# Performance work log

Measured on AMD Instinct MI355X. Metric: run time of the kernel, lower is better.

The kernel has to match this reference:

```python
import jax, jax.numpy as jnp
import numpy as np

A_MIN = 0.001
EPS = 1e-08


def setup_inputs() -> dict:
    key = jax.random.key(0)
    k1, k2, k3, k4 = jax.random.split(key, 4)
    B, O, I = 512, 1024, 512
    x = jax.random.normal(k1, (B, I), dtype=jnp.float32)
    translation = jax.random.uniform(k2, (O, I), dtype=jnp.float32, minval=-1.0, maxval=1.0)
    scale_raw = jax.random.uniform(k3, (O, I), dtype=jnp.float32, minval=-2.0, maxval=0.0)
    weights = jax.random.normal(k4, (O, I), dtype=jnp.float32) * (1.0 / np.sqrt(I))
    return {"x": x, "translation": translation, "scale_raw": scale_raw, "weights": weights}


def reference(x, translation, scale_raw, weights):
    # x: (B, I); params: (O, I)
    scale = A_MIN + jax.nn.softplus(scale_raw)  # (O, I)
    # s: (B, O, I) broadcast intermediate
    s = (x[:, None, :] - translation[None, :, :]) / (scale[None, :, :] + EPS)
    s2 = s * s
    wavelet = (1.0 - s2) * jnp.exp(-0.5 * s2)  # mexican hat
    y = jnp.einsum('oi,boi->bo', weights, wavelet)  # reduce over in_features
    return y
```

## Files before the change

kernel.cpp:

```cpp
#include <hip/hip_runtime.h>


#define WL_A_MIN 0.001f
#define WL_EPS   1e-8f

constexpr int WL_B = 512;
constexpr int WL_O = 1024;
constexpr int WL_I = 512;

#define WL_SQK  0.84932180553704583800f
#define WL_IK   1.38629436111989061883f
#define WL_L2E  1.44269504088896340736f
#define WL_LN2  0.69314718055994530942f

typedef float v2f __attribute__((ext_vector_type(2)));

struct P3 { float nti, inv, w; };

__device__ __forceinline__ float fast_exp2(float a) {
#if __has_builtin(__builtin_amdgcn_exp2f)
    return __builtin_amdgcn_exp2f(a);
#else
    return exp2f(a);
#endif
}
__device__ __forceinline__ float fast_log2(float a) {
#if __has_builtin(__builtin_amdgcn_logf)
    return __builtin_amdgcn_logf(a);
#else
    return __log2f(a);
#endif
}
__device__ __forceinline__ float fast_rcp(float a) {
#if __has_builtin(__builtin_amdgcn_rcpf)
    return __builtin_amdgcn_rcpf(a);
#else
    return 1.0f / a;
#endif
}

__global__ __launch_bounds__(256) void wl_prep(
    const float* __restrict__ translation,
    const float* __restrict__ scale_raw,
    const float* __restrict__ weights,
    v2f* __restrict__ A2,
    float* __restrict__ W1)
{
    __shared__ P3 lds[16 * 64];
    const int t  = threadIdx.x;
    const int o0 = blockIdx.x * 64;
    const int i0 = blockIdx.y * 16;

    {
        const int o_l = t >> 2;
        const int iq  = t & 3;
        const size_t g = (size_t)(o0 + o_l) * WL_I + (i0 + iq * 4);
        const float4 tv = *reinterpret_cast<const float4*>(translation + g);
        const float4 sv = *reinterpret_cast<const float4*>(scale_raw   + g);
        const float4 wv = *reinterpret_cast<const float4*>(weights     + g);
        const float tt[4] = {tv.x, tv.y, tv.z, tv.w};
        const float ss[4] = {sv.x, sv.y, sv.z, sv.w};
        const float ww[4] = {wv.x, wv.y, wv.z, wv.w};
        #pragma unroll
        for (int j = 0; j < 4; ++j) {
            float ex  = fast_exp2(ss[j] * WL_L2E);
            float sp  = fast_log2(1.0f + ex) * WL_LN2;
            float inv = fast_rcp(WL_A_MIN + sp + WL_EPS) * WL_SQK;
            P3 pv; pv.nti = -tt[j] * inv; pv.inv = inv; pv.w = ww[j];
            lds[(iq * 4 + j) * 64 + o_l] = pv;
        }
    }
    __syncthreads();
    {
        const int o_l = t & 63;
        const int r   = t >> 6;
        const int o   = o0 + o_l;
        #pragma unroll
        for (int j = 0; j < 4; ++j) {
            const int i_l = r * 4 + j;
            P3 a = lds[i_l * 64 + o_l];
            A2[(size_t)(i0 + i_l) * WL_O + o] = (v2f){a.nti, a.inv};
            W1[(size_t)(i0 + i_l) * WL_O + o] = a.w;
        }
    }
}

__global__ __launch_bounds__(1024, 8) void wl_main(
    const float* __restrict__ x,
    const v2f* __restrict__ A2,
    const float* __restrict__ W1,
    float* __restrict__ out)
{
    __shared__ float smem[8192];

    const int tid  = threadIdx.x;
    const int lane = tid & 63;
    const int wid  = tid >> 6;
    const int o    = blockIdx.x * 64 + lane;
    const int b0   = blockIdx.y * 16;

    {
        const int b_l = tid & 15;
        const int seg = tid >> 4;
        const float* xg = &x[(size_t)(b0 + b_l) * WL_I + seg * 8];
        const float4 v0 = *reinterpret_cast<const float4*>(xg);
        const float4 v1 = *reinterpret_cast<const float4*>(xg + 4);
        const int base = seg * 8 * 16 + b_l;
        smem[base + 0 * 16] = v0.x;
        smem[base + 1 * 16] = v0.y;
        smem[base + 2 * 16] = v0.z;
        smem[base + 3 * 16] = v0.w;
        smem[base + 4 * 16] = v1.x;
        smem[base + 5 * 16] = v1.y;
        smem[base + 6 * 16] = v1.z;
        smem[base + 7 * 16] = v1.w;
    }
    __syncthreads();

    const v2f*   __restrict__ pA = A2 + (size_t)(wid * 32) * WL_O + o;
    const float* __restrict__ pW = W1 + (size_t)(wid * 32) * WL_O + o;
    const float* xrow = &smem[wid * 32 * 16];

    float acc[16] = {0.f,0.f,0.f,0.f, 0.f,0.f,0.f,0.f,
                     0.f,0.f,0.f,0.f, 0.f,0.f,0.f,0.f};

    #pragma unroll 4
    for (int ii = 0; ii < 32; ++ii) {
        const v2f   pa = pA[(size_t)ii * WL_O];
        const float w  = pW[(size_t)ii * WL_O];
        const float mwk = w * (-WL_IK);
        const float nti = pa.x, inv = pa.y;
        const float4* xf = reinterpret_cast<const float4*>(xrow + ii * 16);
        #pragma unroll
        for (int q = 0; q < 4; ++q) {
            const float4 xq = xf[q];
            const float xs[4] = {xq.x, xq.y, xq.z, xq.w};
            #pragma unroll
            for (int j = 0; j < 4; ++j) {
                const int b = q * 4 + j;
                const float s = fmaf(xs[j], inv, nti);
                const float u = s * s;
                const float e = fast_exp2(-u);
                const float v = fmaf(mwk, u, w);
                acc[b] = fmaf(v, e, acc[b]);
            }
        }
    }

    __syncthreads();
    #pragma unroll
    for (int k = 0; k < 8; ++k)
        smem[(wid * 8 + k) * 64 + lane] = acc[k];
    __syncthreads();
    if (wid < 8) {
        float y = 0.f;
        #pragma unroll
        for (int src = 0; src < 16; ++src)
            y += smem[(src * 8 + wid) * 64 + lane];
        out[(size_t)(b0 + wid) * WL_O + o] = y;
    }
    __syncthreads();
    #pragma unroll
    for (int k = 0; k < 8; ++k)
        smem[(wid * 8 + k) * 64 + lane] = acc[8 + k];
    __syncthreads();
    if (wid >= 8) {
        float y = 0.f;
        #pragma unroll
        for (int src = 0; src < 16; ++src)
            y += smem[(src * 8 + (wid - 8)) * 64 + lane];
        out[(size_t)(b0 + wid) * WL_O + o] = y;
    }
}

extern "C" void kernel_launch(void* const* d_in, const int* in_sizes, int n_in,
                              void* d_out, int out_size, void* d_ws, size_t ws_size,
                              hipStream_t stream) {
    const float* x           = (const float*)d_in[0];
    const float* translation = (const float*)d_in[1];
    const float* scale_raw   = (const float*)d_in[2];
    const float* weights     = (const float*)d_in[3];
    float*       out         = (float*)d_out;
    v2f*   A2 = (v2f*)d_ws;
    float* W1 = (float*)((char*)d_ws + (size_t)WL_I * WL_O * sizeof(v2f));

    wl_prep<<<dim3(WL_O / 64, WL_I / 16), dim3(256), 0, stream>>>(
        translation, scale_raw, weights, A2, W1);

    wl_main<<<dim3(WL_O / 64, WL_B / 16), dim3(1024), 0, stream>>>(
        x, A2, W1, out);
}
```

Before: 104.6 us.

## Pre-transpose x in prep kernel and read it via scalar loads in main

The prep kernel gains 64 extra blocks that transpose x into an (I, B) workspace buffer. The main kernel drops its LDS staging of x and the barrier that followed it, and reads x straight from global memory. The row pointer is made wave-uniform with readfirstlane, so the loads can go through the scalar unit. This removes the per-block x staging and its sync, at the cost of one more transpose pass and of relying on scalar-cache loads inside the inner loop.

```diff
diff --git a/kernel.cpp b/kernel.cpp
--- a/kernel.cpp
+++ b/kernel.cpp
@@ -40,53 +40,90 @@
 }
 
 __global__ __launch_bounds__(256) void wl_prep(
+    const float* __restrict__ x,
     const float* __restrict__ translation,
     const float* __restrict__ scale_raw,
     const float* __restrict__ weights,
     v2f* __restrict__ A2,
-    float* __restrict__ W1)
+    float* __restrict__ W1,
+    float* __restrict__ xT)
 {
-    __shared__ P3 lds[16 * 64];
-    const int t  = threadIdx.x;
-    const int o0 = blockIdx.x * 64;
-    const int i0 = blockIdx.y * 16;
-
-    {
-        const int o_l = t >> 2;
-        const int iq  = t & 3;
-        const size_t g = (size_t)(o0 + o_l) * WL_I + (i0 + iq * 4);
-        const float4 tv = *reinterpret_cast<const float4*>(translation + g);
-        const float4 sv = *reinterpret_cast<const float4*>(scale_raw   + g);
-        const float4 wv = *reinterpret_cast<const float4*>(weights     + g);
-        const float tt[4] = {tv.x, tv.y, tv.z, tv.w};
-        const float ss[4] = {sv.x, sv.y, sv.z, sv.w};
-        const float ww[4] = {wv.x, wv.y, wv.z, wv.w};
-        #pragma unroll
-        for (int j = 0; j < 4; ++j) {
-            float ex  = fast_exp2(ss[j] * WL_L2E);
-            float sp  = fast_log2(1.0f + ex) * WL_LN2;
-            float inv = fast_rcp(WL_A_MIN + sp + WL_EPS) * WL_SQK;
-            P3 pv; pv.nti = -tt[j] * inv; pv.inv = inv; pv.w = ww[j];
-            lds[(iq * 4 + j) * 64 + o_l] = pv;
-        }
-    }
-    __syncthreads();
-    {
-        const int o_l = t & 63;
-        const int r   = t >> 6;
-        const int o   = o0 + o_l;
-        #pragma unroll
-        for (int j = 0; j < 4; ++j) {
-            const int i_l = r * 4 + j;
-            P3 a = lds[i_l * 64 + o_l];
-            A2[(size_t)(i0 + i_l) * WL_O + o] = (v2f){a.nti, a.inv};
-            W1[(size_t)(i0 + i_l) * WL_O + o] = a.w;
+    __shared__ float lds_raw[64 * 65];
+    const int t   = threadIdx.x;
+    const int bid = blockIdx.x;
+
+    if (bid < 512) {
+        P3* lds = reinterpret_cast<P3*>(lds_raw);
+        const int o0 = (bid & 15) * 64;
+        const int i0 = (bid >> 4) * 16;
+        {
+            const int o_l = t >> 2;
+            const int iq  = t & 3;
+            const size_t g = (size_t)(o0 + o_l) * WL_I + (i0 + iq * 4);
+            const float4 tv = *reinterpret_cast<const float4*>(translation + g);
+            const float4 sv = *reinterpret_cast<const float4*>(scale_raw   + g);
+            const float4 wv = *reinterpret_cast<const float4*>(weights     + g);
+            const float tt[4] = {tv.x, tv.y, tv.z, tv.w};
+            const float ss[4] = {sv.x, sv.y, sv.z, sv.w};
+            const float ww[4] = {wv.x, wv.y, wv.z, wv.w};
+            #pragma unroll
+            for (int j = 0; j < 4; ++j) {
+                float ex  = fast_exp2(ss[j] * WL_L2E);
+                float sp  = fast_log2(1.0f + ex) * WL_LN2;
+                float inv = fast_rcp(WL_A_MIN + sp + WL_EPS) * WL_SQK;
+                P3 pv; pv.nti = -tt[j] * inv; pv.inv = inv; pv.w = ww[j];
+                lds[(iq * 4 + j) * 64 + o_l] = pv;
+            }
+        }
+        __syncthreads();
+        {
+            const int o_l = t & 63;
+            const int r   = t >> 6;
+            const int o   = o0 + o_l;
+            #pragma unroll
+            for (int j = 0; j < 4; ++j) {
+                const int i_l = r * 4 + j;
+                P3 a = lds[i_l * 64 + o_l];
+                A2[(size_t)(i0 + i_l) * WL_O + o] = (v2f){a.nti, a.inv};
+                W1[(size_t)(i0 + i_l) * WL_O + o] = a.w;
+            }
+        }
+    } else {
+        float* tile = lds_raw;
+        const int tb = bid - 512;
+        const int ti = tb >> 3, tj = tb & 7;
+        {
+            const int b_l = t >> 2, q = t & 3;
+            const float* src = x + (size_t)(tj * 64 + b_l) * WL_I + ti * 64 + q * 16;
+            #pragma unroll
+            for (int k = 0; k < 4; ++k) {
+                const float4 v = *reinterpret_cast<const float4*>(src + k * 4);
+                const int col = q * 16 + k * 4;
+                tile[b_l * 65 + col + 0] = v.x;
+                tile[b_l * 65 + col + 1] = v.y;
+                tile[b_l * 65 + col + 2] = v.z;
+                tile[b_l * 65 + col + 3] = v.w;
+            }
+        }
+        __syncthreads();
+        {
+            const int i_l = t >> 2, qb = t & 3;
+            float* dst = xT + (size_t)(ti * 64 + i_l) * WL_B + tj * 64 + qb * 16;
+            #pragma unroll
+            for (int k = 0; k < 4; ++k) {
+                float4 v;
+                v.x = tile[(qb * 16 + k * 4 + 0) * 65 + i_l];
+                v.y = tile[(qb * 16 + k * 4 + 1) * 65 + i_l];
+                v.z = tile[(qb * 16 + k * 4 + 2) * 65 + i_l];
+                v.w = tile[(qb * 16 + k * 4 + 3) * 65 + i_l];
+                *reinterpret_cast<float4*>(dst + k * 4) = v;
+            }
         }
     }
 }
 
 __global__ __launch_bounds__(1024, 8) void wl_main(
-    const float* __restrict__ x,
+    const float* __restrict__ xT,
     const v2f* __restrict__ A2,
     const float* __restrict__ W1,
     float* __restrict__ out)
@@ -99,27 +136,11 @@
     const int o    = blockIdx.x * 64 + lane;
     const int b0   = blockIdx.y * 16;
 
-    {
-        const int b_l = tid & 15;
-        const int seg = tid >> 4;
-        const float* xg = &x[(size_t)(b0 + b_l) * WL_I + seg * 8];
-        const float4 v0 = *reinterpret_cast<const float4*>(xg);
-        const float4 v1 = *reinterpret_cast<const float4*>(xg + 4);
-        const int base = seg * 8 * 16 + b_l;
-        smem[base + 0 * 16] = v0.x;
-        smem[base + 1 * 16] = v0.y;
-        smem[base + 2 * 16] = v0.z;
-        smem[base + 3 * 16] = v0.w;
-        smem[base + 4 * 16] = v1.x;
-        smem[base + 5 * 16] = v1.y;
-        smem[base + 6 * 16] = v1.z;
-        smem[base + 7 * 16] = v1.w;
-    }
-    __syncthreads();
+    const int widu = __builtin_amdgcn_readfirstlane(wid);
 
     const v2f*   __restrict__ pA = A2 + (size_t)(wid * 32) * WL_O + o;
     const float* __restrict__ pW = W1 + (size_t)(wid * 32) * WL_O + o;
-    const float* xrow = &smem[wid * 32 * 16];
+    const float* __restrict__ xs = xT + (size_t)(widu * 32) * WL_B + b0;
 
     float acc[16] = {0.f,0.f,0.f,0.f, 0.f,0.f,0.f,0.f,
                      0.f,0.f,0.f,0.f, 0.f,0.f,0.f,0.f};
@@ -130,20 +151,14 @@
         const float w  = pW[(size_t)ii * WL_O];
         const float mwk = w * (-WL_IK);
         const float nti = pa.x, inv = pa.y;
-        const float4* xf = reinterpret_cast<const float4*>(xrow + ii * 16);
+        const float* xrow = xs + (size_t)ii * WL_B;
         #pragma unroll
-        for (int q = 0; q < 4; ++q) {
-            const float4 xq = xf[q];
-            const float xs[4] = {xq.x, xq.y, xq.z, xq.w};
-            #pragma unroll
-            for (int j = 0; j < 4; ++j) {
-                const int b = q * 4 + j;
-                const float s = fmaf(xs[j], inv, nti);
-                const float u = s * s;
-                const float e = fast_exp2(-u);
-                const float v = fmaf(mwk, u, w);
-                acc[b] = fmaf(v, e, acc[b]);
-            }
+        for (int b = 0; b < 16; ++b) {
+            const float s = fmaf(xrow[b], inv, nti);
+            const float u = s * s;
+            const float e = fast_exp2(-u);
+            const float v = fmaf(mwk, u, w);
+            acc[b] = fmaf(v, e, acc[b]);
         }
     }
 
@@ -183,10 +198,11 @@
     float*       out         = (float*)d_out;
     v2f*   A2 = (v2f*)d_ws;
     float* W1 = (float*)((char*)d_ws + (size_t)WL_I * WL_O * sizeof(v2f));
-
-    wl_prep<<<dim3(WL_O / 64, WL_I / 16), dim3(256), 0, stream>>>(
-        translation, scale_raw, weights, A2, W1);
+    float* xT = (float*)((char*)d_ws + (size_t)WL_I * WL_O * (sizeof(v2f) + sizeof(float)));
+
+    wl_prep<<<dim3(576), dim3(256), 0, stream>>>(
+        x, translation, scale_raw, weights, A2, W1, xT);
 
     wl_main<<<dim3(WL_O / 64, WL_B / 16), dim3(1024), 0, stream>>>(
-        x, A2, W1, out);
-}
+        xT, A2, W1, out);
+}
```

New measurement: 104.3 us. About the same (-0.2%).
